# Kernel tuning notes

Measured on AMD Instinct MI355X. Metric: run time of the kernel, lower is better.

The kernel has to match this reference:

```python
import jax, jax.numpy as jnp
import numpy as np

DIM = 1024
B, S = 8, 2048
LN_EPS = 1e-5


def setup_inputs() -> dict:
    key = jax.random.key(0)
    k1, k2, k3 = jax.random.split(key, 3)
    x = jax.random.normal(k1, (B, S, DIM), dtype=jnp.float32)
    # xavier_normal for Linear(dim, 3*dim): std = sqrt(2/(fan_in+fan_out))
    w_qkv = jax.random.normal(k2, (3 * DIM, DIM), dtype=jnp.float32) * np.sqrt(2.0 / (DIM + 3 * DIM))
    w_fc = jax.random.normal(k3, (DIM, DIM), dtype=jnp.float32) * np.sqrt(2.0 / (DIM + DIM))
    b_fc = jnp.zeros((DIM,), dtype=jnp.float32)
    gamma = jnp.ones((DIM,), dtype=jnp.float32)
    beta = jnp.zeros((DIM,), dtype=jnp.float32)
    return {"x": x, "w_qkv": w_qkv, "w_fc": w_fc, "b_fc": b_fc, "gamma": gamma, "beta": beta}


def reference(x, w_qkv, w_fc, b_fc, gamma, beta):
    scaling = DIM ** (-0.5)
    # qkv projection (torch Linear: y = x @ W.T), then chunk into q, k, v
    qkv = jnp.einsum('bsd,ed->bse', x, w_qkv)  # [B, S, 3D]
    q, k, v = jnp.split(qkv, 3, axis=-1)
    # attention scores + softmax over keys
    att = jax.nn.softmax(jnp.einsum('bqd,bkd->bqk', q, k) * scaling, axis=-1)
    # NOTE: faithful to the source einsum 'bqk,bvd->bqd' where k and v are
    # independent summed indices (NOT a standard AV contraction).
    y = jnp.einsum('bqk,bvd->bqd', att, v)
    # fc (dropout is identity in eval mode)
    y = jnp.einsum('bqd,ed->bqe', y, w_fc) + b_fc
    # residual + LayerNorm over last dim
    h = x + y
    mu = jnp.mean(h, axis=-1, keepdims=True)
    var = jnp.var(h, axis=-1, keepdims=True)
    return (h - mu) * jax.lax.rsqrt(var + LN_EPS) * gamma + beta
```

## Files before the change

kernel.cpp:

```cpp
#include <hip/hip_runtime.h>

#define DIM    1024
#define BATCH  8
#define SEQ    2048
#define CHUNKS 64
#define ROWS   (SEQ / CHUNKS)
#define LN_EPS 1e-5f

typedef float v4 __attribute__((ext_vector_type(4)));

__device__ __forceinline__ float dot4(v4 a, v4 b) {
  return a.x * b.x + a.y * b.y + a.z * b.z + a.w * b.w;
}

__global__ __launch_bounds__(256, 4) void k_partial_colsum(
    const float* __restrict__ x, float* __restrict__ partial) {
  const int blk = blockIdx.x;
  const int b = blk >> 6, c = blk & (CHUNKS - 1), t = threadIdx.x;
  const v4* base = (const v4*)x + ((size_t)(b * SEQ + c * ROWS) << 8) + t;
  v4 a0 = {0.f, 0.f, 0.f, 0.f}, a1 = {0.f, 0.f, 0.f, 0.f};
#pragma unroll
  for (int s = 0; s < ROWS; s += 2) {
    a0 += base[(size_t)s << 8];
    a1 += base[(size_t)(s + 1) << 8];
  }
  ((v4*)partial)[((size_t)(c * BATCH + b) << 8) + t] = a0 + a1;
}

__global__ __launch_bounds__(256) void k_finish_colsum(
    const float* __restrict__ partial, float* __restrict__ xsum) {
  const int t = threadIdx.x;
  const int i4 = blockIdx.x * 32 + (t >> 3);
  const int grp = t & 7;
  const int b = i4 >> 8, e4 = i4 & 255;
  const v4* p = (const v4*)partial + ((size_t)b << 8) + e4;
  v4 acc = {0.f, 0.f, 0.f, 0.f};
#pragma unroll
  for (int k = 0; k < 8; ++k)
    acc += p[(size_t)(grp + 8 * k) * (BATCH * 256)];
#pragma unroll
  for (int m = 4; m; m >>= 1) {
    acc.x += __shfl_xor(acc.x, m, 64);
    acc.y += __shfl_xor(acc.y, m, 64);
    acc.z += __shfl_xor(acc.z, m, 64);
    acc.w += __shfl_xor(acc.w, m, 64);
  }
  if (grp == 0) ((v4*)xsum)[i4] = acc;
}

__global__ __launch_bounds__(256) void k_gemv(
    const float* __restrict__ vin, const float* __restrict__ W,
    const float* __restrict__ bias, float* __restrict__ vout) {
  const int wv = threadIdx.x >> 6, lane = threadIdx.x & 63;
  const int o = blockIdx.x * 4 + wv;
  const int b = o >> 10, d = o & (DIM - 1);
  const v4* in4 = (const v4*)vin + ((size_t)b << 8);
  const v4* w4  = (const v4*)W + ((size_t)d << 8);
  float acc = 0.f;
#pragma unroll
  for (int j = 0; j < 4; ++j)
    acc += dot4(w4[lane + 64 * j], in4[lane + 64 * j]);
#pragma unroll
  for (int m = 32; m; m >>= 1) acc += __shfl_xor(acc, m, 64);
  if (lane == 0) {
    float r = acc;
    if (bias) r += bias[d];
    vout[o] = r;
  }
}

__global__ __launch_bounds__(256, 4) void k_residual_ln(
    const float* __restrict__ x, const float* __restrict__ z,
    const float* __restrict__ gamma, const float* __restrict__ beta,
    float* __restrict__ out) {
  __shared__ float zl[DIM];
  const int blk = blockIdx.x, t = threadIdx.x;
  const int wv = t >> 6, lane = t & 63;
  const int b = blk >> 7;

  ((v4*)zl)[t] = ((const v4*)z)[((size_t)b << 8) + t];
  __syncthreads();

  v4 zf[4], gf[4], bf[4];
#pragma unroll
  for (int j = 0; j < 4; ++j) {
    zf[j] = ((const v4*)zl)[lane + 64 * j];
    gf[j] = ((const v4*)gamma)[lane + 64 * j];
    bf[j] = ((const v4*)beta)[lane + 64 * j];
  }

#pragma unroll 1
  for (int r = 0; r < 4; ++r) {
    const int row = (blk << 4) + (wv << 2) + r;
    const v4* xr = (const v4*)x + ((size_t)row << 8);
    v4 h[4];
    float sum = 0.f, ss = 0.f;
#pragma unroll
    for (int j = 0; j < 4; ++j) {
      v4 hv = xr[lane + 64 * j] + zf[j];
      h[j] = hv;
      sum += hv.x + hv.y + hv.z + hv.w;
      ss  += hv.x * hv.x + hv.y * hv.y + hv.z * hv.z + hv.w * hv.w;
    }
#pragma unroll
    for (int m = 32; m; m >>= 1) {
      sum += __shfl_xor(sum, m, 64);
      ss  += __shfl_xor(ss,  m, 64);
    }
    const float inv = 1.0f / (float)DIM;
    const float mu = sum * inv;
    const float rs = rsqrtf(ss * inv - mu * mu + LN_EPS);

    v4* outr = (v4*)out + ((size_t)row << 8);
#pragma unroll
    for (int j = 0; j < 4; ++j)
      outr[lane + 64 * j] = (h[j] - mu) * rs * gf[j] + bf[j];
  }
}

extern "C" void kernel_launch(void* const* d_in, const int* in_sizes, int n_in,
                              void* d_out, int out_size, void* d_ws, size_t ws_size,
                              hipStream_t stream) {
  const float* x     = (const float*)d_in[0];
  const float* w_qkv = (const float*)d_in[1];
  const float* w_fc  = (const float*)d_in[2];
  const float* b_fc  = (const float*)d_in[3];
  const float* gamma = (const float*)d_in[4];
  const float* beta  = (const float*)d_in[5];
  float* out = (float*)d_out;

  float* partial = (float*)d_ws;
  float* xsum    = partial + (size_t)CHUNKS * BATCH * DIM;
  float* vsum    = xsum + (size_t)BATCH * DIM;
  float* z       = vsum + (size_t)BATCH * DIM;

  const float* w_v = w_qkv + (size_t)2 * DIM * DIM;

  hipLaunchKernelGGL(k_partial_colsum, dim3(BATCH * CHUNKS), dim3(256), 0,
                     stream, x, partial);
  hipLaunchKernelGGL(k_finish_colsum, dim3(64), dim3(256), 0, stream,
                     partial, xsum);
  hipLaunchKernelGGL(k_gemv, dim3(BATCH * DIM / 4), dim3(256), 0, stream,
                     xsum, w_v, (const float*)nullptr, vsum);
  hipLaunchKernelGGL(k_gemv, dim3(BATCH * DIM / 4), dim3(256), 0, stream,
                     vsum, w_fc, b_fc, z);
  hipLaunchKernelGGL(k_residual_ln, dim3(BATCH * SEQ / 16), dim3(256), 0,
                     stream, x, z, gamma, beta, out);
}
```

Measured before the change: 47.15 us.

## Fuse all stages into one cooperative persistent kernel with grid barriers

Replaces the five-kernel chain (partial colsum, finish colsum, two GEMVs, residual LayerNorm) with a single cooperative kernel of 512 blocks. The stages are separated by hand-written atomic grid barriers, and the column sums are reduced with float atomicAdd instead of a second pass. This removes four kernel launch gaps and the partial-sum buffer round trip. In exchange it adds a memset launch, three grid-wide spin barriers, and atomic contention. The old multi-kernel path is kept as a fallback if the cooperative launch fails.

```diff
diff --git a/kernel.cpp b/kernel.cpp
--- a/kernel.cpp
+++ b/kernel.cpp
@@ -3,14 +3,206 @@
 #define DIM    1024
 #define BATCH  8
 #define SEQ    2048
+#define NBLK   512
+#define NTHR   256
 #define CHUNKS 64
 #define ROWS   (SEQ / CHUNKS)
 #define LN_EPS 1e-5f
 
 typedef float v4 __attribute__((ext_vector_type(4)));
+typedef unsigned long long u64;
 
 __device__ __forceinline__ float dot4(v4 a, v4 b) {
   return a.x * b.x + a.y * b.y + a.z * b.z + a.w * b.w;
+}
+
+__device__ __forceinline__ float wred(float a) {
+#pragma unroll
+  for (int m = 32; m; m >>= 1) a += __shfl_xor(a, m, 64);
+  return a;
+}
+
+__device__ __forceinline__ void bar_sync(unsigned* cnt, unsigned* flag) {
+  __syncthreads();
+  asm volatile("s_waitcnt vmcnt(0)" ::: "memory");
+  if (threadIdx.x == 0) {
+    unsigned prev = __hip_atomic_fetch_add(cnt, 1u, __ATOMIC_RELAXED,
+                                           __HIP_MEMORY_SCOPE_AGENT);
+    if (prev == NBLK - 1u) {
+      __hip_atomic_store(flag, 1u, __ATOMIC_RELAXED,
+                         __HIP_MEMORY_SCOPE_AGENT);
+    } else {
+      while (__hip_atomic_load(flag, __ATOMIC_RELAXED,
+                               __HIP_MEMORY_SCOPE_AGENT) == 0u)
+        __builtin_amdgcn_s_sleep(8);
+    }
+  }
+  asm volatile("" ::: "memory");
+  __syncthreads();
+}
+
+__global__ __launch_bounds__(NTHR, 4) void k_fused(
+    const float* __restrict__ x, const float* __restrict__ w_v,
+    const float* __restrict__ w_fc, const float* __restrict__ b_fc,
+    const float* __restrict__ gamma, const float* __restrict__ beta,
+    float* __restrict__ out, unsigned* __restrict__ bar,
+    float* __restrict__ xsum, float* __restrict__ vsum,
+    float* __restrict__ z) {
+  __shared__ float smem[DIM];
+  const int blk = blockIdx.x, t = threadIdx.x;
+  const int wv = t >> 6, lane = t & 63;
+  const int b = blk >> 6;
+
+  {
+    const int c = blk & (CHUNKS - 1);
+    const v4* base = (const v4*)x + ((size_t)(b * SEQ + c * ROWS) << 8) + t;
+    v4 a0 = {0.f, 0.f, 0.f, 0.f}, a1 = {0.f, 0.f, 0.f, 0.f};
+#pragma unroll
+    for (int s = 0; s < ROWS; s += 2) {
+      a0 += base[(size_t)s << 8];
+      a1 += base[(size_t)(s + 1) << 8];
+    }
+    v4 a = a0 + a1;
+    float* xp = xsum + (b << 10) + (t << 2);
+    atomicAdd(xp + 0, a.x);
+    atomicAdd(xp + 1, a.y);
+    atomicAdd(xp + 2, a.z);
+    atomicAdd(xp + 3, a.w);
+  }
+  bar_sync(bar + 0, bar + 1);
+
+  {
+    const u64* src = (const u64*)(xsum + (b << 10));
+#pragma unroll
+    for (int k = 0; k < 2; ++k)
+      ((u64*)smem)[t + 256 * k] = __hip_atomic_load(
+          src + t + 256 * k, __ATOMIC_RELAXED, __HIP_MEMORY_SCOPE_AGENT);
+    __syncthreads();
+
+    v4 xf[4];
+#pragma unroll
+    for (int j = 0; j < 4; ++j) xf[j] = ((const v4*)smem)[lane + 64 * j];
+
+    const int obase = blk * 16 + wv * 4;
+    const int dbase = obase & (DIM - 1);
+    v4 w0[4], w1[4], w2[4], w3[4];
+#pragma unroll
+    for (int j = 0; j < 4; ++j) {
+      w0[j] = ((const v4*)w_v + ((size_t)(dbase + 0) << 8))[lane + 64 * j];
+      w1[j] = ((const v4*)w_v + ((size_t)(dbase + 1) << 8))[lane + 64 * j];
+      w2[j] = ((const v4*)w_v + ((size_t)(dbase + 2) << 8))[lane + 64 * j];
+      w3[j] = ((const v4*)w_v + ((size_t)(dbase + 3) << 8))[lane + 64 * j];
+    }
+    float a0 = 0.f, a1 = 0.f, a2 = 0.f, a3 = 0.f;
+#pragma unroll
+    for (int j = 0; j < 4; ++j) {
+      a0 += dot4(w0[j], xf[j]);
+      a1 += dot4(w1[j], xf[j]);
+      a2 += dot4(w2[j], xf[j]);
+      a3 += dot4(w3[j], xf[j]);
+    }
+    a0 = wred(a0); a1 = wred(a1); a2 = wred(a2); a3 = wred(a3);
+    if (lane == 0) {
+      __hip_atomic_store(vsum + obase + 0, a0, __ATOMIC_RELAXED,
+                         __HIP_MEMORY_SCOPE_AGENT);
+      __hip_atomic_store(vsum + obase + 1, a1, __ATOMIC_RELAXED,
+                         __HIP_MEMORY_SCOPE_AGENT);
+      __hip_atomic_store(vsum + obase + 2, a2, __ATOMIC_RELAXED,
+                         __HIP_MEMORY_SCOPE_AGENT);
+      __hip_atomic_store(vsum + obase + 3, a3, __ATOMIC_RELAXED,
+                         __HIP_MEMORY_SCOPE_AGENT);
+    }
+  }
+  bar_sync(bar + 2, bar + 3);
+
+  {
+    const u64* src = (const u64*)(vsum + (b << 10));
+#pragma unroll
+    for (int k = 0; k < 2; ++k)
+      ((u64*)smem)[t + 256 * k] = __hip_atomic_load(
+          src + t + 256 * k, __ATOMIC_RELAXED, __HIP_MEMORY_SCOPE_AGENT);
+    __syncthreads();
+
+    v4 vf[4];
+#pragma unroll
+    for (int j = 0; j < 4; ++j) vf[j] = ((const v4*)smem)[lane + 64 * j];
+
+    const int obase = blk * 16 + wv * 4;
+    const int dbase = obase & (DIM - 1);
+    v4 w0[4], w1[4], w2[4], w3[4];
+#pragma unroll
+    for (int j = 0; j < 4; ++j) {
+      w0[j] = ((const v4*)w_fc + ((size_t)(dbase + 0) << 8))[lane + 64 * j];
+      w1[j] = ((const v4*)w_fc + ((size_t)(dbase + 1) << 8))[lane + 64 * j];
+      w2[j] = ((const v4*)w_fc + ((size_t)(dbase + 2) << 8))[lane + 64 * j];
+      w3[j] = ((const v4*)w_fc + ((size_t)(dbase + 3) << 8))[lane + 64 * j];
+    }
+    float a0 = 0.f, a1 = 0.f, a2 = 0.f, a3 = 0.f;
+#pragma unroll
+    for (int j = 0; j < 4; ++j) {
+      a0 += dot4(w0[j], vf[j]);
+      a1 += dot4(w1[j], vf[j]);
+      a2 += dot4(w2[j], vf[j]);
+      a3 += dot4(w3[j], vf[j]);
+    }
+    a0 = wred(a0); a1 = wred(a1); a2 = wred(a2); a3 = wred(a3);
+    if (lane == 0) {
+      __hip_atomic_store(z + obase + 0, a0 + b_fc[dbase + 0],
+                         __ATOMIC_RELAXED, __HIP_MEMORY_SCOPE_AGENT);
+      __hip_atomic_store(z + obase + 1, a1 + b_fc[dbase + 1],
+                         __ATOMIC_RELAXED, __HIP_MEMORY_SCOPE_AGENT);
+      __hip_atomic_store(z + obase + 2, a2 + b_fc[dbase + 2],
+                         __ATOMIC_RELAXED, __HIP_MEMORY_SCOPE_AGENT);
+      __hip_atomic_store(z + obase + 3, a3 + b_fc[dbase + 3],
+                         __ATOMIC_RELAXED, __HIP_MEMORY_SCOPE_AGENT);
+    }
+  }
+  bar_sync(bar + 4, bar + 5);
+
+  {
+    const u64* src = (const u64*)(z + (b << 10));
+#pragma unroll
+    for (int k = 0; k < 2; ++k)
+      ((u64*)smem)[t + 256 * k] = __hip_atomic_load(
+          src + t + 256 * k, __ATOMIC_RELAXED, __HIP_MEMORY_SCOPE_AGENT);
+    __syncthreads();
+
+    v4 zf[4], gf[4], bf[4];
+#pragma unroll
+    for (int j = 0; j < 4; ++j) {
+      zf[j] = ((const v4*)smem)[lane + 64 * j];
+      gf[j] = ((const v4*)gamma)[lane + 64 * j];
+      bf[j] = ((const v4*)beta)[lane + 64 * j];
+    }
+
+#pragma unroll 1
+    for (int r = 0; r < 8; ++r) {
+      const int row = blk * 32 + wv * 8 + r;
+      const v4* xr = (const v4*)x + ((size_t)row << 8);
+      v4 h[4];
+      float sum = 0.f, ss = 0.f;
+#pragma unroll
+      for (int j = 0; j < 4; ++j) {
+        v4 hv = xr[lane + 64 * j] + zf[j];
+        h[j] = hv;
+        sum += hv.x + hv.y + hv.z + hv.w;
+        ss  += hv.x * hv.x + hv.y * hv.y + hv.z * hv.z + hv.w * hv.w;
+      }
+#pragma unroll
+      for (int m = 32; m; m >>= 1) {
+        sum += __shfl_xor(sum, m, 64);
+        ss  += __shfl_xor(ss,  m, 64);
+      }
+      const float inv = 1.0f / (float)DIM;
+      const float mu = sum * inv;
+      const float rs = rsqrtf(ss * inv - mu * mu + LN_EPS);
+
+      v4* outr = (v4*)out + ((size_t)row << 8);
+#pragma unroll
+      for (int j = 0; j < 4; ++j)
+        outr[lane + 64 * j] = (h[j] - mu) * rs * gf[j] + bf[j];
+    }
+  }
 }
 
 __global__ __launch_bounds__(256, 4) void k_partial_colsum(
@@ -60,8 +252,7 @@
 #pragma unroll
   for (int j = 0; j < 4; ++j)
     acc += dot4(w4[lane + 64 * j], in4[lane + 64 * j]);
-#pragma unroll
-  for (int m = 32; m; m >>= 1) acc += __shfl_xor(acc, m, 64);
+  acc = wred(acc);
   if (lane == 0) {
     float r = acc;
     if (bias) r += bias[d];
@@ -77,10 +268,8 @@
   const int blk = blockIdx.x, t = threadIdx.x;
   const int wv = t >> 6, lane = t & 63;
   const int b = blk >> 7;
-
   ((v4*)zl)[t] = ((const v4*)z)[((size_t)b << 8) + t];
   __syncthreads();
-
   v4 zf[4], gf[4], bf[4];
 #pragma unroll
   for (int j = 0; j < 4; ++j) {
@@ -88,7 +277,6 @@
     gf[j] = ((const v4*)gamma)[lane + 64 * j];
     bf[j] = ((const v4*)beta)[lane + 64 * j];
   }
-
 #pragma unroll 1
   for (int r = 0; r < 4; ++r) {
     const int row = (blk << 4) + (wv << 2) + r;
@@ -110,7 +298,6 @@
     const float inv = 1.0f / (float)DIM;
     const float mu = sum * inv;
     const float rs = rsqrtf(ss * inv - mu * mu + LN_EPS);
-
     v4* outr = (v4*)out + ((size_t)row << 8);
 #pragma unroll
     for (int j = 0; j < 4; ++j)
@@ -129,21 +316,31 @@
   const float* beta  = (const float*)d_in[5];
   float* out = (float*)d_out;
 
-  float* partial = (float*)d_ws;
-  float* xsum    = partial + (size_t)CHUNKS * BATCH * DIM;
-  float* vsum    = xsum + (size_t)BATCH * DIM;
-  float* z       = vsum + (size_t)BATCH * DIM;
+  unsigned* bar  = (unsigned*)d_ws;
+  float* xsum    = (float*)((char*)d_ws + 256);
+  float* vsum    = xsum + BATCH * DIM;
+  float* z       = vsum + BATCH * DIM;
+  float* partial = z + BATCH * DIM;
 
   const float* w_v = w_qkv + (size_t)2 * DIM * DIM;
 
-  hipLaunchKernelGGL(k_partial_colsum, dim3(BATCH * CHUNKS), dim3(256), 0,
-                     stream, x, partial);
-  hipLaunchKernelGGL(k_finish_colsum, dim3(64), dim3(256), 0, stream,
-                     partial, xsum);
-  hipLaunchKernelGGL(k_gemv, dim3(BATCH * DIM / 4), dim3(256), 0, stream,
-                     xsum, w_v, (const float*)nullptr, vsum);
-  hipLaunchKernelGGL(k_gemv, dim3(BATCH * DIM / 4), dim3(256), 0, stream,
-                     vsum, w_fc, b_fc, z);
-  hipLaunchKernelGGL(k_residual_ln, dim3(BATCH * SEQ / 16), dim3(256), 0,
-                     stream, x, z, gamma, beta, out);
-}
+  (void)hipMemsetAsync(d_ws, 0, 256 + BATCH * DIM * sizeof(float), stream);
+
+  void* args[] = {(void*)&x,    (void*)&w_v,   (void*)&w_fc, (void*)&b_fc,
+                  (void*)&gamma, (void*)&beta, (void*)&out,  (void*)&bar,
+                  (void*)&xsum, (void*)&vsum,  (void*)&z};
+  hipError_t err = hipLaunchCooperativeKernel((void*)k_fused, dim3(NBLK),
+                                              dim3(NTHR), args, 0, stream);
+  if (err != hipSuccess) {
+    hipLaunchKernelGGL(k_partial_colsum, dim3(BATCH * CHUNKS), dim3(256), 0,
+                       stream, x, partial);
+    hipLaunchKernelGGL(k_finish_colsum, dim3(64), dim3(256), 0, stream,
+                       partial, xsum);
+    hipLaunchKernelGGL(k_gemv, dim3(BATCH * DIM / 4), dim3(256), 0, stream,
+                       xsum, w_v, (const float*)nullptr, vsum);
+    hipLaunchKernelGGL(k_gemv, dim3(BATCH * DIM / 4), dim3(256), 0, stream,
+                       vsum, w_fc, b_fc, z);
+    hipLaunchKernelGGL(k_residual_ln, dim3(BATCH * SEQ / 16), dim3(256), 0,
+                       stream, x, z, gamma, beta, out);
+  }
+}
```

New measurement: 126.5 us. +168.3%, slower.
